# Optimization experiments

Hardware: AMD Instinct MI355X
Metric: run time of the kernel (lower is better)

## Reference

```python
import jax, jax.numpy as jnp
import numpy as np

B, K, D = 16, 1024, 512
HS = 2048   # shared_hidden
HR = 1024   # routed_hidden
E = 8       # num_routed


def setup_inputs() -> dict:
    key = jax.random.key(0)
    ks = jax.random.split(key, 16)
    s = 0.02
    x = jax.random.normal(ks[0], (B, K, D), dtype=jnp.float32)
    # routing probabilities: positive, row-normalized (softmax'd upstream in the original)
    rw = jax.random.uniform(ks[1], (B, E), dtype=jnp.float32)
    rw = rw / jnp.sum(rw, axis=-1, keepdims=True)
    return {
        "x": x,
        "routing_weights": rw,
        # shared SwiGLU params
        "Ws_gate": jax.random.normal(ks[2], (D, HS), dtype=jnp.float32) * s,
        "bs_gate": jnp.zeros((HS,), dtype=jnp.float32),
        "Ws_up": jax.random.normal(ks[3], (D, HS), dtype=jnp.float32) * s,
        "bs_up": jnp.zeros((HS,), dtype=jnp.float32),
        "Ws_down": jax.random.normal(ks[4], (HS, D), dtype=jnp.float32) * s,
        "bs_down": jnp.zeros((D,), dtype=jnp.float32),
        # routed SwiGLU params, stacked over experts
        "Wr_gate": jax.random.normal(ks[5], (E, D, HR), dtype=jnp.float32) * s,
        "br_gate": jnp.zeros((E, HR), dtype=jnp.float32),
        "Wr_up": jax.random.normal(ks[6], (E, D, HR), dtype=jnp.float32) * s,
        "br_up": jnp.zeros((E, HR), dtype=jnp.float32),
        "Wr_down": jax.random.normal(ks[7], (E, HR, D), dtype=jnp.float32) * s,
        "br_down": jnp.zeros((E, D), dtype=jnp.float32),
    }


def reference(x, routing_weights,
              Ws_gate, bs_gate, Ws_up, bs_up, Ws_down, bs_down,
              Wr_gate, br_gate, Wr_up, br_up, Wr_down, br_down):
    # shared SwiGLU (dropout is identity at eval)
    h_s = jax.nn.silu(x @ Ws_gate + bs_gate) * (x @ Ws_up + bs_up)  # [B,K,HS]
    shared_out = h_s @ Ws_down + bs_down                             # [B,K,D]

    # routed experts: dense soft routing (hard_route=False path)
    g = jnp.einsum('bkd,edh->bekh', x, Wr_gate) + br_gate[None, :, None, :]  # [B,E,K,HR]
    u = jnp.einsum('bkd,edh->bekh', x, Wr_up) + br_up[None, :, None, :]      # [B,E,K,HR]
    h_r = jax.nn.silu(g) * u                                                 # [B,E,K,HR]
    out_e = jnp.einsum('bekh,ehd->bekd', h_r, Wr_down) + br_down[None, :, None, :]  # [B,E,K,D]
    routed_out = jnp.einsum('bekd,be->bkd', out_e, routing_weights)          # [B,K,D]

    return shared_out + routed_out
```

## Files before the change

### kernel.cpp

```cpp
#include <hip/hip_runtime.h>

typedef __bf16 bf16_t;
typedef bf16_t bf16x8 __attribute__((ext_vector_type(8)));
typedef float f32x4 __attribute__((ext_vector_type(4)));

__device__ inline f32x4 mfma16(bf16x8 a, bf16x8 b, f32x4 c) {
    return __builtin_amdgcn_mfma_f32_16x16x32_bf16(a, b, c, 0, 0, 0);
}

__device__ inline ushort f2bf(float f) {
    unsigned u = __builtin_bit_cast(unsigned, f);
    unsigned r = (u + 0x7FFFu + ((u >> 16) & 1u)) >> 16;
    return (ushort)r;
}

__device__ inline void gload_lds16(const void* g, void* l) {
    __builtin_amdgcn_global_load_lds(
        (const __attribute__((address_space(1))) void*)g,
        (__attribute__((address_space(3))) void*)l, 16, 0, 0);
}

#define M_TOT 16384
#define N_UNITS 10
#define UNIT_W (1024*512)

__global__ void k_cvt_x(const float* __restrict__ x, ushort* __restrict__ xb) {
    int i = (blockIdx.x * 256 + threadIdx.x) * 4;
    float4 v = *reinterpret_cast<const float4*>(x + i);
    ushort4 o;
    o.x = f2bf(v.x); o.y = f2bf(v.y); o.z = f2bf(v.z); o.w = f2bf(v.w);
    *reinterpret_cast<ushort4*>(xb + i) = o;
}

template<int ROWS, int COLS, int MODE>
__global__ void k_trans(const float* __restrict__ Wsh, const float* __restrict__ Wrt,
                        ushort* __restrict__ dst) {
    int u = blockIdx.z;
    const float* src; int stride;
    if (MODE == 0) {
        if (u < 2) { src = Wsh + u * COLS; stride = 2 * COLS; }
        else       { src = Wrt + (size_t)(u - 2) * ROWS * COLS; stride = COLS; }
    } else {
        src = (u < 2) ? (Wsh + (size_t)u * ROWS * COLS)
                      : (Wrt + (size_t)(u - 2) * ROWS * COLS);
        stride = COLS;
    }
    __shared__ float t[64][65];
    int r0 = blockIdx.y * 64, c0 = blockIdx.x * 64;
    int tid = threadIdx.x;
#pragma unroll
    for (int i = 0; i < 16; ++i) {
        int idx = i * 256 + tid;
        int r = idx >> 6, c = idx & 63;
        t[r][c] = src[(r0 + r) * stride + c0 + c];
    }
    __syncthreads();
    ushort* d = dst + (size_t)u * ROWS * COLS;
#pragma unroll
    for (int i = 0; i < 16; ++i) {
        int idx = i * 256 + tid;
        int r = idx >> 6, c = idx & 63;
        d[(c0 + r) * ROWS + (r0 + c)] = f2bf(t[c][r]);
    }
}

__global__ __launch_bounds__(256, 2) void gemm_gateup2(
    const ushort* __restrict__ A, const ushort* __restrict__ WG, const ushort* __restrict__ WU,
    const float* __restrict__ bsg, const float* __restrict__ bsu,
    const float* __restrict__ brg, const float* __restrict__ bru,
    const float* __restrict__ rw, ushort* __restrict__ Hall,
    int unit_base, int m_base, int mc, int log2p) {
    __shared__ ushort lsA[128 * 64];
    __shared__ ushort lsG[128 * 64];
    __shared__ ushort lsU[128 * 64];
    const int nwg = gridDim.x, cpx = nwg >> 3;
    const int lid = blockIdx.x;
    const int swz = (lid & 7) * cpx + (lid >> 3);
    const int ul = swz >> log2p;
    const int rem = swz & ((1 << log2p) - 1);
    const int bm = (rem >> 3) * 128;
    const int bn = (rem & 7) * 128;
    const int ug = unit_base + ul;
    const ushort* Bg = WG + (size_t)ug * UNIT_W;
    const ushort* Bu = WU + (size_t)ug * UNIT_W;

    const int tid = threadIdx.x;
    const int l = tid & 63, w = tid >> 6;
    const int wm = w >> 1, wn = w & 1;

    f32x4 accg[4][4] = {};
    f32x4 accu[4][4] = {};

    for (int kk = 0; kk < 512; kk += 64) {
#pragma unroll
        for (int j = 0; j < 4; ++j) {
            int q = w * 4 + j;
            int c = q * 64 + l;
            int row = c >> 3, pc = c & 7;
            int lc = pc ^ (row & 7);
            int koff = kk + lc * 8;
            gload_lds16(A  + (size_t)(m_base + bm + row) * 512 + koff, lsA + q * 512);
            gload_lds16(Bg + (size_t)(bn + row) * 512 + koff,          lsG + q * 512);
            gload_lds16(Bu + (size_t)(bn + row) * 512 + koff,          lsU + q * 512);
        }
        __syncthreads();
#pragma unroll
        for (int s = 0; s < 2; ++s) {
            bf16x8 af[4], gf[4], uf[4];
#pragma unroll
            for (int i = 0; i < 4; ++i) {
                int ar = wm * 64 + i * 16 + (l & 15);
                int br = wn * 64 + i * 16 + (l & 15);
                int lcr = s * 4 + (l >> 4);
                af[i] = *reinterpret_cast<const bf16x8*>(&lsA[ar * 64 + ((lcr ^ (ar & 7)) * 8)]);
                gf[i] = *reinterpret_cast<const bf16x8*>(&lsG[br * 64 + ((lcr ^ (br & 7)) * 8)]);
                uf[i] = *reinterpret_cast<const bf16x8*>(&lsU[br * 64 + ((lcr ^ (br & 7)) * 8)]);
            }
#pragma unroll
            for (int mi = 0; mi < 4; ++mi)
#pragma unroll
                for (int ni = 0; ni < 4; ++ni) {
                    accg[mi][ni] = mfma16(af[mi], gf[ni], accg[mi][ni]);
                    accu[mi][ni] = mfma16(af[mi], uf[ni], accu[mi][ni]);
                }
        }
        __syncthreads();
    }

    const float* bg = (ug < 2) ? (bsg + ug * 1024) : (brg + (ug - 2) * 1024);
    const float* bu = (ug < 2) ? (bsu + ug * 1024) : (bru + (ug - 2) * 1024);
    const float scale = (ug < 2) ? 1.0f : rw[((m_base + bm) >> 10) * 8 + (ug - 2)];
    ushort* H = Hall + (size_t)ul * mc * 1024;
#pragma unroll
    for (int ni = 0; ni < 4; ++ni) {
        int col = bn + wn * 64 + ni * 16 + (l & 15);
        float bgv = bg[col], buv = bu[col];
#pragma unroll
        for (int mi = 0; mi < 4; ++mi)
#pragma unroll
            for (int r = 0; r < 4; ++r) {
                int lrow = bm + wm * 64 + mi * 16 + (l >> 4) * 4 + r;
                float g = accg[mi][ni][r] + bgv;
                float uu = accu[mi][ni][r] + buv;
                float h = g / (1.0f + __expf(-g)) * uu * scale;
                H[(size_t)lrow * 1024 + col] = f2bf(h);
            }
    }
}

template<int TN>
__global__ __launch_bounds__(256, 2) void gemm_down2(
    const ushort* __restrict__ Hall, const ushort* __restrict__ WD,
    const float* __restrict__ bsd, const float* __restrict__ brd,
    const float* __restrict__ rw, float* __restrict__ out,
    int nu, int unit_base, int m_base, int mc, int accumulate) {
    constexpr int WN = TN / 2;
    constexpr int NI = WN / 16;
    constexpr int BCH = TN / 32;
    constexpr int NBN = 512 / TN;
    __shared__ ushort lsA[128 * 64];
    __shared__ ushort lsB[TN * 64];
    const int nwg = gridDim.x, cpx = nwg >> 3;
    const int lid = blockIdx.x;
    const int swz = (lid & 7) * cpx + (lid >> 3);
    const int bm = (swz / NBN) * 128;
    const int bn = (swz % NBN) * TN;

    const int tid = threadIdx.x;
    const int l = tid & 63, w = tid >> 6;
    const int wm = w >> 1, wn = w & 1;

    f32x4 acc[4][NI] = {};

    for (int u = 0; u < nu; ++u) {
        const ushort* Au = Hall + (size_t)u * mc * 1024;
        const ushort* Bu = WD + (size_t)(unit_base + u) * UNIT_W;
        for (int kk = 0; kk < 1024; kk += 64) {
#pragma unroll
            for (int j = 0; j < 4; ++j) {
                int q = w * 4 + j;
                int c = q * 64 + l;
                int row = c >> 3, pc = c & 7;
                int lc = pc ^ (row & 7);
                gload_lds16(Au + (size_t)(bm + row) * 1024 + kk + lc * 8, lsA + q * 512);
            }
#pragma unroll
            for (int j = 0; j < BCH; ++j) {
                int q = w * BCH + j;
                int c = q * 64 + l;
                int row = c >> 3, pc = c & 7;
                int lc = pc ^ (row & 7);
                gload_lds16(Bu + (size_t)(bn + row) * 1024 + kk + lc * 8, lsB + q * 512);
            }
            __syncthreads();
#pragma unroll
            for (int s = 0; s < 2; ++s) {
                bf16x8 af[4], bfr[NI];
#pragma unroll
                for (int i = 0; i < 4; ++i) {
                    int ar = wm * 64 + i * 16 + (l & 15);
                    int lcr = s * 4 + (l >> 4);
                    af[i] = *reinterpret_cast<const bf16x8*>(&lsA[ar * 64 + ((lcr ^ (ar & 7)) * 8)]);
                }
#pragma unroll
                for (int i = 0; i < NI; ++i) {
                    int br = wn * WN + i * 16 + (l & 15);
                    int lcr = s * 4 + (l >> 4);
                    bfr[i] = *reinterpret_cast<const bf16x8*>(&lsB[br * 64 + ((lcr ^ (br & 7)) * 8)]);
                }
#pragma unroll
                for (int mi = 0; mi < 4; ++mi)
#pragma unroll
                    for (int ni = 0; ni < NI; ++ni)
                        acc[mi][ni] = mfma16(af[mi], bfr[ni], acc[mi][ni]);
            }
            __syncthreads();
        }
    }

    const int b = (m_base + bm) >> 10;
#pragma unroll
    for (int ni = 0; ni < NI; ++ni) {
        int col = bn + wn * WN + ni * 16 + (l & 15);
        float bias = 0.0f;
        if (!accumulate) {
            bias = bsd[col];
#pragma unroll
            for (int e = 0; e < 8; ++e)
                bias += rw[b * 8 + e] * brd[e * 512 + col];
        }
#pragma unroll
        for (int mi = 0; mi < 4; ++mi)
#pragma unroll
            for (int r = 0; r < 4; ++r) {
                int grow = m_base + bm + wm * 64 + mi * 16 + (l >> 4) * 4 + r;
                if (accumulate) out[(size_t)grow * 512 + col] += acc[mi][ni][r];
                else            out[(size_t)grow * 512 + col]  = acc[mi][ni][r] + bias;
            }
    }
}

extern "C" void kernel_launch(void* const* d_in, const int* in_sizes, int n_in,
                              void* d_out, int out_size, void* d_ws, size_t ws_size,
                              hipStream_t stream) {
    const float* x   = (const float*)d_in[0];
    const float* rw  = (const float*)d_in[1];
    const float* Wsg = (const float*)d_in[2];
    const float* bsg = (const float*)d_in[3];
    const float* Wsu = (const float*)d_in[4];
    const float* bsu = (const float*)d_in[5];
    const float* Wsd = (const float*)d_in[6];
    const float* bsd = (const float*)d_in[7];
    const float* Wrg = (const float*)d_in[8];
    const float* brg = (const float*)d_in[9];
    const float* Wru = (const float*)d_in[10];
    const float* bru = (const float*)d_in[11];
    const float* Wrd = (const float*)d_in[12];
    const float* brd = (const float*)d_in[13];
    float* out = (float*)d_out;

    const size_t xb_b = (size_t)M_TOT * 512 * 2;
    const size_t w_b  = (size_t)N_UNITS * UNIT_W * 2;

    char* ws = (char*)d_ws;
    ushort* xb  = (ushort*)ws; ws += xb_b;
    ushort* wgT = (ushort*)ws; ws += w_b;
    ushort* wuT = (ushort*)ws; ws += w_b;
    ushort* wdT = (ushort*)ws; ws += w_b;
    ushort* Hb  = (ushort*)ws;

    const size_t base_b = xb_b + 3 * w_b;
    const size_t hall16 = (size_t)N_UNITS * 16384 * 1024 * 2;
    const size_t hall8  = (size_t)N_UNITS * 8192 * 1024 * 2;

    k_cvt_x<<<8192, 256, 0, stream>>>(x, xb);
    k_trans<512, 1024, 0><<<dim3(16, 8, 10), 256, 0, stream>>>(Wsg, Wrg, wgT);
    k_trans<512, 1024, 0><<<dim3(16, 8, 10), 256, 0, stream>>>(Wsu, Wru, wuT);
    k_trans<1024, 512, 1><<<dim3(8, 16, 10), 256, 0, stream>>>(Wsd, Wrd, wdT);

    if (ws_size >= base_b + hall16) {
        gemm_gateup2<<<10240, 256, 0, stream>>>(xb, wgT, wuT, bsg, bsu, brg, bru, rw, Hb,
                                                0, 0, 16384, 10);
        gemm_down2<128><<<512, 256, 0, stream>>>(Hb, wdT, bsd, brd, rw, out,
                                                 N_UNITS, 0, 0, 16384, 0);
    } else if (ws_size >= base_b + hall8) {
        for (int ch = 0; ch < 2; ++ch) {
            gemm_gateup2<<<5120, 256, 0, stream>>>(xb, wgT, wuT, bsg, bsu, brg, bru, rw, Hb,
                                                   0, ch * 8192, 8192, 9);
            gemm_down2<64><<<512, 256, 0, stream>>>(Hb, wdT, bsd, brd, rw, out,
                                                    N_UNITS, 0, ch * 8192, 8192, 0);
        }
    } else {
        for (int u = 0; u < N_UNITS; ++u) {
            gemm_gateup2<<<1024, 256, 0, stream>>>(xb, wgT, wuT, bsg, bsu, brg, bru, rw, Hb,
                                                   u, 0, 16384, 10);
            gemm_down2<128><<<512, 256, 0, stream>>>(Hb, wdT, bsd, brd, rw, out,
                                                     1, u, 0, 16384, u > 0 ? 1 : 0);
        }
    }
}
```

Before: 759.5 us.

## Interleave gate/up weights into one matrix and split experts into two groups

Gate and up weight columns are interleaved in 16-wide blocks into a single 2048-wide matrix, so each gate-up tile runs one GEMM whose accumulator holds matching gate and up columns. This frees registers and LDS compared with keeping two separate B tiles and two accumulator sets. The schedule becomes two groups of five units, each doing gate-up then a down-projection that accumulates into the output, so the intermediate buffer is half size. The down GEMM now uses 64-wide N tiles across 1024 blocks. The trade-off is an extra read-modify-write of the output in the second group and smaller down tiles.

```diff
diff --git a/kernel.cpp b/kernel.cpp
--- a/kernel.cpp
+++ b/kernel.cpp
@@ -23,6 +23,7 @@
 #define M_TOT 16384
 #define N_UNITS 10
 #define UNIT_W (1024*512)
+#define UNIT_W2 (2048*512)
 
 __global__ void k_cvt_x(const float* __restrict__ x, ushort* __restrict__ xb) {
     int i = (blockIdx.x * 256 + threadIdx.x) * 4;
@@ -32,19 +33,13 @@
     *reinterpret_cast<ushort4*>(xb + i) = o;
 }
 
-template<int ROWS, int COLS, int MODE>
-__global__ void k_trans(const float* __restrict__ Wsh, const float* __restrict__ Wrt,
-                        ushort* __restrict__ dst) {
+template<int IS_UP>
+__global__ void k_trans2(const float* __restrict__ Wsh, const float* __restrict__ Wrt,
+                         ushort* __restrict__ W2) {
     int u = blockIdx.z;
     const float* src; int stride;
-    if (MODE == 0) {
-        if (u < 2) { src = Wsh + u * COLS; stride = 2 * COLS; }
-        else       { src = Wrt + (size_t)(u - 2) * ROWS * COLS; stride = COLS; }
-    } else {
-        src = (u < 2) ? (Wsh + (size_t)u * ROWS * COLS)
-                      : (Wrt + (size_t)(u - 2) * ROWS * COLS);
-        stride = COLS;
-    }
+    if (u < 2) { src = Wsh + u * 1024; stride = 2048; }
+    else       { src = Wrt + (size_t)(u - 2) * 512 * 1024; stride = 1024; }
     __shared__ float t[64][65];
     int r0 = blockIdx.y * 64, c0 = blockIdx.x * 64;
     int tid = threadIdx.x;
@@ -55,41 +50,65 @@
         t[r][c] = src[(r0 + r) * stride + c0 + c];
     }
     __syncthreads();
-    ushort* d = dst + (size_t)u * ROWS * COLS;
+    ushort* d = W2 + (size_t)u * UNIT_W2;
 #pragma unroll
     for (int i = 0; i < 16; ++i) {
         int idx = i * 256 + tid;
         int r = idx >> 6, c = idx & 63;
-        d[(c0 + r) * ROWS + (r0 + c)] = f2bf(t[c][r]);
-    }
-}
-
-__global__ __launch_bounds__(256, 2) void gemm_gateup2(
-    const ushort* __restrict__ A, const ushort* __restrict__ WG, const ushort* __restrict__ WU,
+        int rc = c0 + r;
+        int n = ((rc >> 4) << 5) + IS_UP * 16 + (rc & 15);
+        d[(size_t)n * 512 + (r0 + c)] = f2bf(t[c][r]);
+    }
+}
+
+template<int ROWS, int COLS>
+__global__ void k_transD(const float* __restrict__ Wsh, const float* __restrict__ Wrt,
+                         ushort* __restrict__ dst) {
+    int u = blockIdx.z;
+    const float* src = (u < 2) ? (Wsh + (size_t)u * ROWS * COLS)
+                               : (Wrt + (size_t)(u - 2) * ROWS * COLS);
+    int stride = COLS;
+    __shared__ float t[64][65];
+    int r0 = blockIdx.y * 64, c0 = blockIdx.x * 64;
+    int tid = threadIdx.x;
+#pragma unroll
+    for (int i = 0; i < 16; ++i) {
+        int idx = i * 256 + tid;
+        int r = idx >> 6, c = idx & 63;
+        t[r][c] = src[(r0 + r) * stride + c0 + c];
+    }
+    __syncthreads();
+    ushort* d = dst + (size_t)u * ROWS * COLS;
+#pragma unroll
+    for (int i = 0; i < 16; ++i) {
+        int idx = i * 256 + tid;
+        int r = idx >> 6, c = idx & 63;
+        d[(size_t)(c0 + r) * ROWS + (r0 + c)] = f2bf(t[c][r]);
+    }
+}
+
+__global__ __launch_bounds__(256, 2) void gemm_gu3(
+    const ushort* __restrict__ A, const ushort* __restrict__ W2,
     const float* __restrict__ bsg, const float* __restrict__ bsu,
     const float* __restrict__ brg, const float* __restrict__ bru,
-    const float* __restrict__ rw, ushort* __restrict__ Hall,
-    int unit_base, int m_base, int mc, int log2p) {
+    const float* __restrict__ rw, ushort* __restrict__ Hall, int unit_base) {
     __shared__ ushort lsA[128 * 64];
-    __shared__ ushort lsG[128 * 64];
-    __shared__ ushort lsU[128 * 64];
+    __shared__ ushort lsB[128 * 64];
     const int nwg = gridDim.x, cpx = nwg >> 3;
     const int lid = blockIdx.x;
     const int swz = (lid & 7) * cpx + (lid >> 3);
-    const int ul = swz >> log2p;
-    const int rem = swz & ((1 << log2p) - 1);
-    const int bm = (rem >> 3) * 128;
-    const int bn = (rem & 7) * 128;
+    const int ul = swz >> 11;
+    const int rem = swz & 2047;
+    const int bm = (rem >> 4) * 128;
+    const int bnc = (rem & 15) * 128;
     const int ug = unit_base + ul;
-    const ushort* Bg = WG + (size_t)ug * UNIT_W;
-    const ushort* Bu = WU + (size_t)ug * UNIT_W;
+    const ushort* Bw = W2 + (size_t)ug * UNIT_W2;
 
     const int tid = threadIdx.x;
     const int l = tid & 63, w = tid >> 6;
     const int wm = w >> 1, wn = w & 1;
 
-    f32x4 accg[4][4] = {};
-    f32x4 accu[4][4] = {};
+    f32x4 acc[4][4] = {};
 
     for (int kk = 0; kk < 512; kk += 64) {
 #pragma unroll
@@ -99,81 +118,72 @@
             int row = c >> 3, pc = c & 7;
             int lc = pc ^ (row & 7);
             int koff = kk + lc * 8;
-            gload_lds16(A  + (size_t)(m_base + bm + row) * 512 + koff, lsA + q * 512);
-            gload_lds16(Bg + (size_t)(bn + row) * 512 + koff,          lsG + q * 512);
-            gload_lds16(Bu + (size_t)(bn + row) * 512 + koff,          lsU + q * 512);
+            gload_lds16(A  + (size_t)(bm + row) * 512 + koff,  lsA + q * 512);
+            gload_lds16(Bw + (size_t)(bnc + row) * 512 + koff, lsB + q * 512);
         }
         __syncthreads();
 #pragma unroll
         for (int s = 0; s < 2; ++s) {
-            bf16x8 af[4], gf[4], uf[4];
+            bf16x8 af[4], bf[4];
+            int lcr = s * 4 + (l >> 4);
 #pragma unroll
             for (int i = 0; i < 4; ++i) {
                 int ar = wm * 64 + i * 16 + (l & 15);
                 int br = wn * 64 + i * 16 + (l & 15);
-                int lcr = s * 4 + (l >> 4);
                 af[i] = *reinterpret_cast<const bf16x8*>(&lsA[ar * 64 + ((lcr ^ (ar & 7)) * 8)]);
-                gf[i] = *reinterpret_cast<const bf16x8*>(&lsG[br * 64 + ((lcr ^ (br & 7)) * 8)]);
-                uf[i] = *reinterpret_cast<const bf16x8*>(&lsU[br * 64 + ((lcr ^ (br & 7)) * 8)]);
+                bf[i] = *reinterpret_cast<const bf16x8*>(&lsB[br * 64 + ((lcr ^ (br & 7)) * 8)]);
             }
 #pragma unroll
             for (int mi = 0; mi < 4; ++mi)
 #pragma unroll
-                for (int ni = 0; ni < 4; ++ni) {
-                    accg[mi][ni] = mfma16(af[mi], gf[ni], accg[mi][ni]);
-                    accu[mi][ni] = mfma16(af[mi], uf[ni], accu[mi][ni]);
-                }
+                for (int ni = 0; ni < 4; ++ni)
+                    acc[mi][ni] = mfma16(af[mi], bf[ni], acc[mi][ni]);
         }
         __syncthreads();
     }
 
     const float* bg = (ug < 2) ? (bsg + ug * 1024) : (brg + (ug - 2) * 1024);
     const float* bu = (ug < 2) ? (bsu + ug * 1024) : (bru + (ug - 2) * 1024);
-    const float scale = (ug < 2) ? 1.0f : rw[((m_base + bm) >> 10) * 8 + (ug - 2)];
-    ushort* H = Hall + (size_t)ul * mc * 1024;
-#pragma unroll
-    for (int ni = 0; ni < 4; ++ni) {
-        int col = bn + wn * 64 + ni * 16 + (l & 15);
-        float bgv = bg[col], buv = bu[col];
+    const float scale = (ug < 2) ? 1.0f : rw[(bm >> 10) * 8 + (ug - 2)];
+    ushort* H = Hall + (size_t)ul * M_TOT * 1024;
+#pragma unroll
+    for (int p = 0; p < 2; ++p) {
+        int colH = ((bnc + wn * 64) >> 1) + p * 16 + (l & 15);
+        float bgv = bg[colH], buv = bu[colH];
 #pragma unroll
         for (int mi = 0; mi < 4; ++mi)
 #pragma unroll
             for (int r = 0; r < 4; ++r) {
-                int lrow = bm + wm * 64 + mi * 16 + (l >> 4) * 4 + r;
-                float g = accg[mi][ni][r] + bgv;
-                float uu = accu[mi][ni][r] + buv;
+                int row = bm + wm * 64 + mi * 16 + (l >> 4) * 4 + r;
+                float g = acc[mi][2 * p][r] + bgv;
+                float uu = acc[mi][2 * p + 1][r] + buv;
                 float h = g / (1.0f + __expf(-g)) * uu * scale;
-                H[(size_t)lrow * 1024 + col] = f2bf(h);
-            }
-    }
-}
-
-template<int TN>
-__global__ __launch_bounds__(256, 2) void gemm_down2(
+                H[(size_t)row * 1024 + colH] = f2bf(h);
+            }
+    }
+}
+
+__global__ __launch_bounds__(256, 2) void gemm_dn3(
     const ushort* __restrict__ Hall, const ushort* __restrict__ WD,
     const float* __restrict__ bsd, const float* __restrict__ brd,
     const float* __restrict__ rw, float* __restrict__ out,
-    int nu, int unit_base, int m_base, int mc, int accumulate) {
-    constexpr int WN = TN / 2;
-    constexpr int NI = WN / 16;
-    constexpr int BCH = TN / 32;
-    constexpr int NBN = 512 / TN;
+    int nu, int unit_base, int accumulate) {
     __shared__ ushort lsA[128 * 64];
-    __shared__ ushort lsB[TN * 64];
+    __shared__ ushort lsB[64 * 64];
     const int nwg = gridDim.x, cpx = nwg >> 3;
     const int lid = blockIdx.x;
     const int swz = (lid & 7) * cpx + (lid >> 3);
-    const int bm = (swz / NBN) * 128;
-    const int bn = (swz % NBN) * TN;
+    const int bm = (swz >> 3) * 128;
+    const int bn = (swz & 7) * 64;
 
     const int tid = threadIdx.x;
     const int l = tid & 63, w = tid >> 6;
     const int wm = w >> 1, wn = w & 1;
 
-    f32x4 acc[4][NI] = {};
+    f32x4 acc[4][2] = {};
 
     for (int u = 0; u < nu; ++u) {
-        const ushort* Au = Hall + (size_t)u * mc * 1024;
+        const ushort* Au = Hall + (size_t)u * M_TOT * 1024;
         const ushort* Bu = WD + (size_t)(unit_base + u) * UNIT_W;
         for (int kk = 0; kk < 1024; kk += 64) {
 #pragma unroll
@@ -185,8 +195,8 @@
                 gload_lds16(Au + (size_t)(bm + row) * 1024 + kk + lc * 8, lsA + q * 512);
             }
 #pragma unroll
-            for (int j = 0; j < BCH; ++j) {
-                int q = w * BCH + j;
+            for (int j = 0; j < 2; ++j) {
+                int q = w * 2 + j;
                 int c = q * 64 + l;
                 int row = c >> 3, pc = c & 7;
                 int lc = pc ^ (row & 7);
@@ -195,33 +205,32 @@
             __syncthreads();
 #pragma unroll
             for (int s = 0; s < 2; ++s) {
-                bf16x8 af[4], bfr[NI];
+                bf16x8 af[4], bfr[2];
+                int lcr = s * 4 + (l >> 4);
 #pragma unroll
                 for (int i = 0; i < 4; ++i) {
                     int ar = wm * 64 + i * 16 + (l & 15);
-                    int lcr = s * 4 + (l >> 4);
                     af[i] = *reinterpret_cast<const bf16x8*>(&lsA[ar * 64 + ((lcr ^ (ar & 7)) * 8)]);
                 }
 #pragma unroll
-                for (int i = 0; i < NI; ++i) {
-                    int br = wn * WN + i * 16 + (l & 15);
-                    int lcr = s * 4 + (l >> 4);
+                for (int i = 0; i < 2; ++i) {
+                    int br = wn * 32 + i * 16 + (l & 15);
                     bfr[i] = *reinterpret_cast<const bf16x8*>(&lsB[br * 64 + ((lcr ^ (br & 7)) * 8)]);
                 }
 #pragma unroll
                 for (int mi = 0; mi < 4; ++mi)
 #pragma unroll
-                    for (int ni = 0; ni < NI; ++ni)
+                    for (int ni = 0; ni < 2; ++ni)
                         acc[mi][ni] = mfma16(af[mi], bfr[ni], acc[mi][ni]);
             }
             __syncthreads();
         }
     }
 
-    const int b = (m_base + bm) >> 10;
-#pragma unroll
-    for (int ni = 0; ni < NI; ++ni) {
-        int col = bn + wn * WN + ni * 16 + (l & 15);
+    const int b = bm >> 10;
+#pragma unroll
+    for (int ni = 0; ni < 2; ++ni) {
+        int col = bn + wn * 32 + ni * 16 + (l & 15);
         float bias = 0.0f;
         if (!accumulate) {
             bias = bsd[col];
@@ -233,7 +242,7 @@
         for (int mi = 0; mi < 4; ++mi)
 #pragma unroll
             for (int r = 0; r < 4; ++r) {
-                int grow = m_base + bm + wm * 64 + mi * 16 + (l >> 4) * 4 + r;
+                int grow = bm + wm * 64 + mi * 16 + (l >> 4) * 4 + r;
                 if (accumulate) out[(size_t)grow * 512 + col] += acc[mi][ni][r];
                 else            out[(size_t)grow * 512 + col]  = acc[mi][ni][r] + bias;
             }
@@ -259,43 +268,34 @@
     const float* brd = (const float*)d_in[13];
     float* out = (float*)d_out;
 
-    const size_t xb_b = (size_t)M_TOT * 512 * 2;
-    const size_t w_b  = (size_t)N_UNITS * UNIT_W * 2;
+    const size_t xb_b  = (size_t)M_TOT * 512 * 2;
+    const size_t w2_b  = (size_t)N_UNITS * UNIT_W2 * 2;
+    const size_t wd_b  = (size_t)N_UNITS * UNIT_W * 2;
 
     char* ws = (char*)d_ws;
     ushort* xb  = (ushort*)ws; ws += xb_b;
-    ushort* wgT = (ushort*)ws; ws += w_b;
-    ushort* wuT = (ushort*)ws; ws += w_b;
-    ushort* wdT = (ushort*)ws; ws += w_b;
+    ushort* W2  = (ushort*)ws; ws += w2_b;
+    ushort* wdT = (ushort*)ws; ws += wd_b;
     ushort* Hb  = (ushort*)ws;
 
-    const size_t base_b = xb_b + 3 * w_b;
-    const size_t hall16 = (size_t)N_UNITS * 16384 * 1024 * 2;
-    const size_t hall8  = (size_t)N_UNITS * 8192 * 1024 * 2;
+    const size_t base_b = xb_b + w2_b + wd_b;
+    const size_t hall5 = (size_t)5 * M_TOT * 1024 * 2;
+    const size_t hall1 = (size_t)M_TOT * 1024 * 2;
 
     k_cvt_x<<<8192, 256, 0, stream>>>(x, xb);
-    k_trans<512, 1024, 0><<<dim3(16, 8, 10), 256, 0, stream>>>(Wsg, Wrg, wgT);
-    k_trans<512, 1024, 0><<<dim3(16, 8, 10), 256, 0, stream>>>(Wsu, Wru, wuT);
-    k_trans<1024, 512, 1><<<dim3(8, 16, 10), 256, 0, stream>>>(Wsd, Wrd, wdT);
-
-    if (ws_size >= base_b + hall16) {
-        gemm_gateup2<<<10240, 256, 0, stream>>>(xb, wgT, wuT, bsg, bsu, brg, bru, rw, Hb,
-                                                0, 0, 16384, 10);
-        gemm_down2<128><<<512, 256, 0, stream>>>(Hb, wdT, bsd, brd, rw, out,
-                                                 N_UNITS, 0, 0, 16384, 0);
-    } else if (ws_size >= base_b + hall8) {
-        for (int ch = 0; ch < 2; ++ch) {
-            gemm_gateup2<<<5120, 256, 0, stream>>>(xb, wgT, wuT, bsg, bsu, brg, bru, rw, Hb,
-                                                   0, ch * 8192, 8192, 9);
-            gemm_down2<64><<<512, 256, 0, stream>>>(Hb, wdT, bsd, brd, rw, out,
-                                                    N_UNITS, 0, ch * 8192, 8192, 0);
+    k_trans2<0><<<dim3(16, 8, 10), 256, 0, stream>>>(Wsg, Wrg, W2);
+    k_trans2<1><<<dim3(16, 8, 10), 256, 0, stream>>>(Wsu, Wru, W2);
+    k_transD<1024, 512><<<dim3(8, 16, 10), 256, 0, stream>>>(Wsd, Wrd, wdT);
+
+    if (ws_size >= base_b + hall5) {
+        for (int g = 0; g < 2; ++g) {
+            gemm_gu3<<<10240, 256, 0, stream>>>(xb, W2, bsg, bsu, brg, bru, rw, Hb, g * 5);
+            gemm_dn3<<<1024, 256, 0, stream>>>(Hb, wdT, bsd, brd, rw, out, 5, g * 5, g);
         }
     } else {
         for (int u = 0; u < N_UNITS; ++u) {
-            gemm_gateup2<<<1024, 256, 0, stream>>>(xb, wgT, wuT, bsg, bsu, brg, bru, rw, Hb,
-                                                   u, 0, 16384, 10);
-            gemm_down2<128><<<512, 256, 0, stream>>>(Hb, wdT, bsd, brd, rw, out,
-                                                     1, u, 0, 16384, u > 0 ? 1 : 0);
-        }
-    }
-}
+            gemm_gu3<<<2048, 256, 0, stream>>>(xb, W2, bsg, bsu, brg, bru, rw, Hb, u);
+            gemm_dn3<<<1024, 256, 0, stream>>>(Hb, wdT, bsd, brd, rw, out, 1, u, u > 0 ? 1 : 0);
+        }
+    }
+}
```

New measurement: 703.7 us. 7.3% less time.
